# Kernel tuning notes

Hardware: AMD Instinct MI355X
Metric: run time of the kernel (lower is better)

The kernel has to match this reference:

```python
import jax, jax.numpy as jnp
import numpy as np

D_MODEL = 1024
N_HEADS = 16
D_K = D_MODEL // N_HEADS
B, S = 4, 2048


def setup_inputs() -> dict:
    key = jax.random.key(0)
    ks = jax.random.split(key, 9)
    sc = 1.0 / np.sqrt(D_MODEL)
    return {
        "x": jax.random.normal(ks[0], (B, S, D_MODEL), dtype=jnp.float32),
        "Wq": jax.random.normal(ks[1], (D_MODEL, D_MODEL), dtype=jnp.float32) * sc,
        "bq": jax.random.normal(ks[2], (D_MODEL,), dtype=jnp.float32) * 0.02,
        "Wk": jax.random.normal(ks[3], (D_MODEL, D_MODEL), dtype=jnp.float32) * sc,
        "bk": jax.random.normal(ks[4], (D_MODEL,), dtype=jnp.float32) * 0.02,
        "Wv": jax.random.normal(ks[5], (D_MODEL, D_MODEL), dtype=jnp.float32) * sc,
        "bv": jax.random.normal(ks[6], (D_MODEL,), dtype=jnp.float32) * 0.02,
        "Wo": jax.random.normal(ks[7], (D_MODEL, D_MODEL), dtype=jnp.float32) * sc,
        "bo": jax.random.normal(ks[8], (D_MODEL,), dtype=jnp.float32) * 0.02,
    }


def reference(x, Wq, bq, Wk, bk, Wv, bv, Wo, bo):
    b, s, _ = x.shape
    # QKV projections (torch Linear: x @ W.T + b; here weights are stored as [in, out])
    q = (x @ Wq + bq).reshape(b, s, N_HEADS, D_K).transpose(0, 2, 1, 3)  # [b,h,s,dk]
    k = (x @ Wk + bk).reshape(b, s, N_HEADS, D_K).transpose(0, 2, 1, 3)
    v = (x @ Wv + bv).reshape(b, s, N_HEADS, D_K).transpose(0, 2, 1, 3)
    scores = jnp.einsum("bhqd,bhkd->bhqk", q, k) / jnp.sqrt(jnp.float32(D_K))
    attn = jax.nn.softmax(scores, axis=-1)  # dropout=0.0 -> identity
    out = jnp.einsum("bhqk,bhkd->bhqd", attn, v)
    out = out.transpose(0, 2, 1, 3).reshape(b, s, D_MODEL)
    return out @ Wo + bo
```

## Files before the change

### kernel.cpp

```cpp
#include <hip/hip_runtime.h>
#include <hip/hip_bf16.h>

#define DM    1024
#define NH    16
#define DKH   64
#define BB    4
#define SS    2048
#define MROWS (BB*SS)
#define NQK   2048

typedef __attribute__((ext_vector_type(8))) __bf16 bf16x8;
typedef __attribute__((ext_vector_type(4))) float f32x4;
typedef __attribute__((ext_vector_type(4))) unsigned short u16x4;

__device__ __forceinline__ void gload_lds16(const void* g, void* l) {
  __builtin_amdgcn_global_load_lds((const __attribute__((address_space(1))) void*)g,
                                   (__attribute__((address_space(3))) void*)l, 16, 0, 0);
}

__device__ __forceinline__ unsigned short f2bf(float f) {
  __hip_bfloat16 h = __float2bfloat16(f);
  unsigned short u;
  __builtin_memcpy(&u, &h, 2);
  return u;
}


__global__ __launch_bounds__(256) void cvt_bf16_kernel(const float* __restrict__ in,
                                                       unsigned short* __restrict__ out, int n4) {
  int i = blockIdx.x * 256 + threadIdx.x;
  if (i >= n4) return;
  float4 v = reinterpret_cast<const float4*>(in)[i];
  u16x4 o = { f2bf(v.x), f2bf(v.y), f2bf(v.z), f2bf(v.w) };
  reinterpret_cast<u16x4*>(out)[i] = o;
}

__global__ __launch_bounds__(256) void transpose_cvt_kernel(const float* __restrict__ W,
                                                            unsigned short* __restrict__ WT) {
  __shared__ float t[32][33];
  int tx = threadIdx.x & 31, ty = threadIdx.x >> 5;
  int bx = blockIdx.x * 32, by = blockIdx.y * 32;
#pragma unroll
  for (int i = 0; i < 32; i += 8)
    t[ty + i][tx] = W[(long)(by + ty + i) * DM + bx + tx];
  __syncthreads();
#pragma unroll
  for (int i = 0; i < 32; i += 8)
    WT[(long)(bx + ty + i) * DM + by + tx] = f2bf(t[tx][ty + i]);
}

__global__ void concat2_bias_kernel(const float* __restrict__ a, const float* __restrict__ b,
                                    float* __restrict__ out) {
  int i = blockIdx.x * 256 + threadIdx.x;
  if (i >= NQK) return;
  out[i] = (i < DM) ? a[i] : b[i - DM];
}


__device__ __forceinline__ void store_out(float* p, float v) { *p = v; }
__device__ __forceinline__ void store_out(unsigned short* p, float v) { *p = f2bf(v); }

template <typename OutT, bool Q_SCALE, bool BIAS_ROW>
__global__ __launch_bounds__(256) void gemm_bt_kernel(
    const unsigned short* __restrict__ A,
    const unsigned short* __restrict__ BT,
    const float* __restrict__ bias,
    OutT* __restrict__ C, int M, int N, int K) {
  __shared__ unsigned short As[128 * 32];
  __shared__ unsigned short Bs[128 * 32];
  const int tid = threadIdx.x;
  const int lane = tid & 63;
  const int lr = lane & 15, lg = lane >> 4;
  const int wv = tid >> 6, wm = wv >> 1, wn = wv & 1;
  const long bm = blockIdx.x, bn = blockIdx.y;

  const unsigned short* Ag = A + bm * 128 * K;
  const unsigned short* Bg = BT + bn * 128 * K;

  f32x4 acc[4][4];
#pragma unroll
  for (int i = 0; i < 4; ++i)
#pragma unroll
    for (int j = 0; j < 4; ++j) acc[i][j] = (f32x4){0.f, 0.f, 0.f, 0.f};

  for (int kt = 0; kt < K; kt += 32) {
#pragma unroll
    for (int it = 0; it < 2; ++it) {
      const int e = it * 2048 + tid * 8;
      const int row = e >> 5, col = e & 31;
      gload_lds16(Ag + (long)row * K + kt + col, As + e);
      gload_lds16(Bg + (long)row * K + kt + col, Bs + e);
    }
    __syncthreads();
    bf16x8 af[4], bfr[4];
#pragma unroll
    for (int mi = 0; mi < 4; ++mi)
      af[mi] = *reinterpret_cast<const bf16x8*>(As + (wm * 64 + mi * 16 + lr) * 32 + lg * 8);
#pragma unroll
    for (int ni = 0; ni < 4; ++ni)
      bfr[ni] = *reinterpret_cast<const bf16x8*>(Bs + (wn * 64 + ni * 16 + lr) * 32 + lg * 8);
#pragma unroll
    for (int mi = 0; mi < 4; ++mi)
#pragma unroll
      for (int ni = 0; ni < 4; ++ni)
        acc[mi][ni] = __builtin_amdgcn_mfma_f32_16x16x32_bf16(af[mi], bfr[ni], acc[mi][ni], 0, 0, 0);
    __syncthreads();
  }

#pragma unroll
  for (int ni = 0; ni < 4; ++ni) {
    const int col = (int)bn * 128 + wn * 64 + ni * 16 + lr;
    const float bc = BIAS_ROW ? 0.f : bias[col];
    const float sc = (Q_SCALE && col < DM) ? (0.125f * 1.44269504088896340736f) : 1.0f;
#pragma unroll
    for (int mi = 0; mi < 4; ++mi) {
      const long row0 = bm * 128 + wm * 64 + mi * 16 + lg * 4;
#pragma unroll
      for (int r = 0; r < 4; ++r) {
        const float bv = BIAS_ROW ? bias[row0 + r] : bc;
        float v = (acc[mi][ni][r] + bv) * sc;
        store_out(&C[(row0 + r) * (long)N + col], v);
      }
    }
  }
}


__global__ __launch_bounds__(256) void attn_kernel(
    const unsigned short* __restrict__ QK,
    const unsigned short* __restrict__ Vt,
    unsigned short* __restrict__ AO) {
  __shared__ unsigned short Ks[2][64 * 64];
  __shared__ unsigned short Vs[2][64 * 64];
  __shared__ unsigned short Pl[4][16 * 64];

  const int tid = threadIdx.x;
  const int lane = tid & 63;
  const int wv = tid >> 6;
  const int lr = lane & 15, lg = lane >> 4;

  const int bh = blockIdx.x;
  const int qt = blockIdx.y;
  const int b = bh >> 4, h = bh & 15;

  const unsigned short* Qp = QK + (long)b * SS * NQK + h * DKH;
  const unsigned short* Kp = Qp + DM;
  const unsigned short* Vp = Vt + (long)h * DKH * MROWS + (long)b * SS;

  bf16x8 qf[2][2];
#pragma unroll
  for (int f = 0; f < 2; ++f) {
    const unsigned short* qrow = Qp + (long)(qt * 128 + wv * 32 + f * 16 + lr) * NQK;
    qf[f][0] = *reinterpret_cast<const bf16x8*>(qrow + lg * 8);
    qf[f][1] = *reinterpret_cast<const bf16x8*>(qrow + 32 + lg * 8);
  }

  f32x4 acc[2][4];
#pragma unroll
  for (int f = 0; f < 2; ++f)
#pragma unroll
    for (int d = 0; d < 4; ++d) acc[f][d] = (f32x4){0.f, 0.f, 0.f, 0.f};
  float m_run[2] = {-1e30f, -1e30f};
  float l_run[2] = {0.f, 0.f};

  unsigned short* Pw = &Pl[wv][0];

  auto stage = [&](int bf, int t) {
#pragma unroll
    for (int it = 0; it < 2; ++it) {
      const int s = it * 256 + tid;
      const int row = s >> 3, blk = s & 7;
      const int blkL = blk ^ (row & 7);
      gload_lds16(Kp + (long)(t * 64 + row) * NQK + (blkL << 3), &Ks[bf][s * 8]);
      gload_lds16(Vp + (long)row * MROWS + t * 64 + (blkL << 3), &Vs[bf][s * 8]);
    }
  };

  stage(0, 0);
  __syncthreads();

  const int NT = SS / 64;
  for (int kt = 0; kt < NT; ++kt) {
    const int cur = kt & 1;
    if (kt + 1 < NT) stage(cur ^ 1, kt + 1);

    f32x4 s4[2][4];
#pragma unroll
    for (int f = 0; f < 2; ++f)
#pragma unroll
      for (int kb = 0; kb < 4; ++kb) s4[f][kb] = (f32x4){0.f, 0.f, 0.f, 0.f};
    __builtin_amdgcn_s_setprio(1);
#pragma unroll
    for (int kb = 0; kb < 4; ++kb) {
      const unsigned short* kbase = &Ks[cur][(kb * 16 + lr) * 64];
      bf16x8 kf0 = *reinterpret_cast<const bf16x8*>(kbase + ((lg ^ (lr & 7)) << 3));
      bf16x8 kf1 = *reinterpret_cast<const bf16x8*>(kbase + (((4 + lg) ^ (lr & 7)) << 3));
      s4[0][kb] = __builtin_amdgcn_mfma_f32_16x16x32_bf16(kf0, qf[0][0], s4[0][kb], 0, 0, 0);
      s4[0][kb] = __builtin_amdgcn_mfma_f32_16x16x32_bf16(kf1, qf[0][1], s4[0][kb], 0, 0, 0);
      s4[1][kb] = __builtin_amdgcn_mfma_f32_16x16x32_bf16(kf0, qf[1][0], s4[1][kb], 0, 0, 0);
      s4[1][kb] = __builtin_amdgcn_mfma_f32_16x16x32_bf16(kf1, qf[1][1], s4[1][kb], 0, 0, 0);
    }
    __builtin_amdgcn_s_setprio(0);

    bf16x8 pf[2][2];
    float scl[2];
#pragma unroll
    for (int f = 0; f < 2; ++f) {
      float mloc = s4[f][0][0];
#pragma unroll
      for (int kb = 0; kb < 4; ++kb)
#pragma unroll
        for (int r = 0; r < 4; ++r) mloc = fmaxf(mloc, s4[f][kb][r]);
      mloc = fmaxf(mloc, __shfl_xor(mloc, 16));
      mloc = fmaxf(mloc, __shfl_xor(mloc, 32));
      const float mn = fmaxf(m_run[f], mloc);
      scl[f] = __builtin_amdgcn_exp2f(m_run[f] - mn);
      m_run[f] = mn;
      float ssum = 0.f;
#pragma unroll
      for (int kb = 0; kb < 4; ++kb) {
        u16x4 pw;
#pragma unroll
        for (int r = 0; r < 4; ++r) {
          float p = __builtin_amdgcn_exp2f(s4[f][kb][r] - mn);
          ssum += p;
          pw[r] = f2bf(p);
        }
        *reinterpret_cast<u16x4*>(Pw + lr * 64 + ((((kb * 4 + lg) ^ ((lr & 7) << 1))) << 2)) = pw;
      }
      ssum += __shfl_xor(ssum, 16);
      ssum += __shfl_xor(ssum, 32);
      l_run[f] = l_run[f] * scl[f] + ssum;
      pf[f][0] = *reinterpret_cast<const bf16x8*>(Pw + lr * 64 + (((lg * 2) ^ ((lr & 7) << 1)) << 2));
      pf[f][1] = *reinterpret_cast<const bf16x8*>(Pw + lr * 64 + (((8 + lg * 2) ^ ((lr & 7) << 1)) << 2));
    }

#pragma unroll
    for (int f = 0; f < 2; ++f)
#pragma unroll
      for (int d = 0; d < 4; ++d)
#pragma unroll
        for (int r = 0; r < 4; ++r) acc[f][d][r] *= scl[f];

    __builtin_amdgcn_s_setprio(1);
#pragma unroll
    for (int dblk = 0; dblk < 4; ++dblk) {
      const unsigned short* vbase = &Vs[cur][(dblk * 16 + lr) * 64];
      bf16x8 vf0 = *reinterpret_cast<const bf16x8*>(vbase + ((lg ^ (lr & 7)) << 3));
      bf16x8 vf1 = *reinterpret_cast<const bf16x8*>(vbase + (((4 + lg) ^ (lr & 7)) << 3));
      acc[0][dblk] = __builtin_amdgcn_mfma_f32_16x16x32_bf16(vf0, pf[0][0], acc[0][dblk], 0, 0, 0);
      acc[0][dblk] = __builtin_amdgcn_mfma_f32_16x16x32_bf16(vf1, pf[0][1], acc[0][dblk], 0, 0, 0);
      acc[1][dblk] = __builtin_amdgcn_mfma_f32_16x16x32_bf16(vf0, pf[1][0], acc[1][dblk], 0, 0, 0);
      acc[1][dblk] = __builtin_amdgcn_mfma_f32_16x16x32_bf16(vf1, pf[1][1], acc[1][dblk], 0, 0, 0);
    }
    __builtin_amdgcn_s_setprio(0);

    __syncthreads();
  }

#pragma unroll
  for (int f = 0; f < 2; ++f) {
    const float inv = 1.0f / l_run[f];
    const long row = (long)b * SS + qt * 128 + wv * 32 + f * 16 + lr;
#pragma unroll
    for (int dblk = 0; dblk < 4; ++dblk) {
      u16x4 o;
#pragma unroll
      for (int r = 0; r < 4; ++r) o[r] = f2bf(acc[f][dblk][r] * inv);
      *reinterpret_cast<u16x4*>(AO + row * DM + h * DKH + dblk * 16 + lg * 4) = o;
    }
  }
}


extern "C" void kernel_launch(void* const* d_in, const int* in_sizes, int n_in,
                              void* d_out, int out_size, void* d_ws, size_t ws_size,
                              hipStream_t stream) {
  const float* x  = (const float*)d_in[0];
  const float* Wq = (const float*)d_in[1];
  const float* bq = (const float*)d_in[2];
  const float* Wk = (const float*)d_in[3];
  const float* bk = (const float*)d_in[4];
  const float* Wv = (const float*)d_in[5];
  const float* bv = (const float*)d_in[6];
  const float* Wo = (const float*)d_in[7];
  const float* bo = (const float*)d_in[8];
  float* out = (float*)d_out;

  char* ws = (char*)d_ws;
  size_t off = 0;
  auto alloc = [&](size_t bytes) {
    void* p = ws + off;
    off += (bytes + 255) & ~(size_t)255;
    return p;
  };
  unsigned short* Xb   = (unsigned short*)alloc((size_t)MROWS * DM * 2);
  unsigned short* WTqk = (unsigned short*)alloc((size_t)2 * DM * DM * 2);
  unsigned short* WTv  = (unsigned short*)alloc((size_t)DM * DM * 2);
  unsigned short* WTo  = (unsigned short*)alloc((size_t)DM * DM * 2);
  float*          bqk  = (float*)alloc((size_t)NQK * 4);
  unsigned short* QKb  = (unsigned short*)alloc((size_t)MROWS * NQK * 2);
  unsigned short* Vtb  = (unsigned short*)alloc((size_t)DM * MROWS * 2);
  unsigned short* AOb  = (unsigned short*)alloc((size_t)MROWS * DM * 2);

  cvt_bf16_kernel<<<(MROWS * DM / 4 + 255) / 256, 256, 0, stream>>>(x, Xb, MROWS * DM / 4);
  transpose_cvt_kernel<<<dim3(32, 32), 256, 0, stream>>>(Wq, WTqk);
  transpose_cvt_kernel<<<dim3(32, 32), 256, 0, stream>>>(Wk, WTqk + DM * DM);
  transpose_cvt_kernel<<<dim3(32, 32), 256, 0, stream>>>(Wv, WTv);
  transpose_cvt_kernel<<<dim3(32, 32), 256, 0, stream>>>(Wo, WTo);
  concat2_bias_kernel<<<(NQK + 255) / 256, 256, 0, stream>>>(bq, bk, bqk);

  gemm_bt_kernel<unsigned short, true, false><<<dim3(MROWS / 128, NQK / 128), 256, 0, stream>>>(
      Xb, WTqk, bqk, QKb, MROWS, NQK, DM);
  gemm_bt_kernel<unsigned short, false, true><<<dim3(DM / 128, MROWS / 128), 256, 0, stream>>>(
      WTv, Xb, bv, Vtb, DM, MROWS, DM);

  attn_kernel<<<dim3(BB * NH, SS / 128), 256, 0, stream>>>(QKb, Vtb, AOb);

  gemm_bt_kernel<float, false, false><<<dim3(MROWS / 128, DM / 128), 256, 0, stream>>>(
      AOb, WTo, bo, out, MROWS, DM, DM);
}
```

Measured before the change: 259.3 us.

## Switch attention to 32x32x16 MFMA with register-shuffled P and lazy rescale

Rewrites the attention inner loop around 32x32x16 bf16 MFMAs instead of 16x16x32. The P tile is passed from the QK^T output layout to the PV operand layout with cross-lane shuffles rather than a round trip through LDS. K/V tiles are now stored in LDS in a k-major block layout with no XOR swizzle. Rescaling of the accumulator is skipped unless the row max grows by more than a threshold, which removes most per-tile rescale work but lets exp values grow up to 2^8 before normalization.

```diff
diff --git a/kernel.cpp b/kernel.cpp
--- a/kernel.cpp
+++ b/kernel.cpp
@@ -11,6 +11,7 @@
 
 typedef __attribute__((ext_vector_type(8))) __bf16 bf16x8;
 typedef __attribute__((ext_vector_type(4))) float f32x4;
+typedef __attribute__((ext_vector_type(16))) float f32x16;
 typedef __attribute__((ext_vector_type(4))) unsigned short u16x4;
 
 __device__ __forceinline__ void gload_lds16(const void* g, void* l) {
@@ -23,6 +24,10 @@
   unsigned short u;
   __builtin_memcpy(&u, &h, 2);
   return u;
+}
+
+__device__ __forceinline__ unsigned pack2(float a, float b) {
+  return (unsigned)f2bf(a) | ((unsigned)f2bf(b) << 16);
 }
 
 
@@ -130,14 +135,15 @@
     const unsigned short* __restrict__ QK,
     const unsigned short* __restrict__ Vt,
     unsigned short* __restrict__ AO) {
-  __shared__ unsigned short Ks[2][64 * 64];
-  __shared__ unsigned short Vs[2][64 * 64];
-  __shared__ unsigned short Pl[4][16 * 64];
+  __shared__ __align__(16) unsigned char smem[32768];
+  unsigned short* KsB = (unsigned short*)smem;
+  unsigned short* VsB = (unsigned short*)(smem + 16384);
 
   const int tid = threadIdx.x;
   const int lane = tid & 63;
   const int wv = tid >> 6;
-  const int lr = lane & 15, lg = lane >> 4;
+  const int q5 = lane & 31;
+  const int hi = lane >> 5;
 
   const int bh = blockIdx.x;
   const int qt = blockIdx.y;
@@ -147,32 +153,29 @@
   const unsigned short* Kp = Qp + DM;
   const unsigned short* Vp = Vt + (long)h * DKH * MROWS + (long)b * SS;
 
-  bf16x8 qf[2][2];
-#pragma unroll
-  for (int f = 0; f < 2; ++f) {
-    const unsigned short* qrow = Qp + (long)(qt * 128 + wv * 32 + f * 16 + lr) * NQK;
-    qf[f][0] = *reinterpret_cast<const bf16x8*>(qrow + lg * 8);
-    qf[f][1] = *reinterpret_cast<const bf16x8*>(qrow + 32 + lg * 8);
+  bf16x8 qf[4];
+  {
+    const unsigned short* qrow = Qp + (long)(qt * 128 + wv * 32 + q5) * NQK;
+#pragma unroll
+    for (int dstep = 0; dstep < 4; ++dstep)
+      qf[dstep] = *reinterpret_cast<const bf16x8*>(qrow + dstep * 16 + hi * 8);
   }
 
-  f32x4 acc[2][4];
-#pragma unroll
-  for (int f = 0; f < 2; ++f)
-#pragma unroll
-    for (int d = 0; d < 4; ++d) acc[f][d] = (f32x4){0.f, 0.f, 0.f, 0.f};
-  float m_run[2] = {-1e30f, -1e30f};
-  float l_run[2] = {0.f, 0.f};
-
-  unsigned short* Pw = &Pl[wv][0];
-
-  auto stage = [&](int bf, int t) {
+  f32x16 accv[2];
+#pragma unroll
+  for (int d = 0; d < 2; ++d)
+#pragma unroll
+    for (int r = 0; r < 16; ++r) accv[d][r] = 0.f;
+  float m_run = -1e30f, l_run = 0.f;
+
+  auto stage = [&](int buf, int t) {
+    unsigned short* kd = KsB + buf * 4096;
+    unsigned short* vd = VsB + buf * 4096;
 #pragma unroll
     for (int it = 0; it < 2; ++it) {
-      const int s = it * 256 + tid;
-      const int row = s >> 3, blk = s & 7;
-      const int blkL = blk ^ (row & 7);
-      gload_lds16(Kp + (long)(t * 64 + row) * NQK + (blkL << 3), &Ks[bf][s * 8]);
-      gload_lds16(Vp + (long)row * MROWS + t * 64 + (blkL << 3), &Vs[bf][s * 8]);
+      const int u = it * 256 + tid;
+      gload_lds16(Kp + (long)(t * 64 + (u & 63)) * NQK + (u >> 6) * 8, kd + u * 8);
+      gload_lds16(Vp + (long)(u & 63) * MROWS + t * 64 + (u >> 6) * 8, vd + u * 8);
     }
   };
 
@@ -183,93 +186,98 @@
   for (int kt = 0; kt < NT; ++kt) {
     const int cur = kt & 1;
     if (kt + 1 < NT) stage(cur ^ 1, kt + 1);
-
-    f32x4 s4[2][4];
-#pragma unroll
-    for (int f = 0; f < 2; ++f)
-#pragma unroll
-      for (int kb = 0; kb < 4; ++kb) s4[f][kb] = (f32x4){0.f, 0.f, 0.f, 0.f};
+    const unsigned short* K_ = KsB + cur * 4096;
+    const unsigned short* V_ = VsB + cur * 4096;
+
+    f32x16 s4[2];
+#pragma unroll
+    for (int kb = 0; kb < 2; ++kb)
+#pragma unroll
+      for (int r = 0; r < 16; ++r) s4[kb][r] = 0.f;
     __builtin_amdgcn_s_setprio(1);
 #pragma unroll
-    for (int kb = 0; kb < 4; ++kb) {
-      const unsigned short* kbase = &Ks[cur][(kb * 16 + lr) * 64];
-      bf16x8 kf0 = *reinterpret_cast<const bf16x8*>(kbase + ((lg ^ (lr & 7)) << 3));
-      bf16x8 kf1 = *reinterpret_cast<const bf16x8*>(kbase + (((4 + lg) ^ (lr & 7)) << 3));
-      s4[0][kb] = __builtin_amdgcn_mfma_f32_16x16x32_bf16(kf0, qf[0][0], s4[0][kb], 0, 0, 0);
-      s4[0][kb] = __builtin_amdgcn_mfma_f32_16x16x32_bf16(kf1, qf[0][1], s4[0][kb], 0, 0, 0);
-      s4[1][kb] = __builtin_amdgcn_mfma_f32_16x16x32_bf16(kf0, qf[1][0], s4[1][kb], 0, 0, 0);
-      s4[1][kb] = __builtin_amdgcn_mfma_f32_16x16x32_bf16(kf1, qf[1][1], s4[1][kb], 0, 0, 0);
-    }
+    for (int kb = 0; kb < 2; ++kb)
+#pragma unroll
+      for (int dstep = 0; dstep < 4; ++dstep) {
+        bf16x8 kf = *reinterpret_cast<const bf16x8*>(
+            K_ + ((dstep * 2 + hi) * 64 + kb * 32 + q5) * 8);
+        s4[kb] = __builtin_amdgcn_mfma_f32_32x32x16_bf16(kf, qf[dstep], s4[kb], 0, 0, 0);
+      }
     __builtin_amdgcn_s_setprio(0);
 
-    bf16x8 pf[2][2];
-    float scl[2];
-#pragma unroll
-    for (int f = 0; f < 2; ++f) {
-      float mloc = s4[f][0][0];
-#pragma unroll
-      for (int kb = 0; kb < 4; ++kb)
-#pragma unroll
-        for (int r = 0; r < 4; ++r) mloc = fmaxf(mloc, s4[f][kb][r]);
-      mloc = fmaxf(mloc, __shfl_xor(mloc, 16));
-      mloc = fmaxf(mloc, __shfl_xor(mloc, 32));
-      const float mn = fmaxf(m_run[f], mloc);
-      scl[f] = __builtin_amdgcn_exp2f(m_run[f] - mn);
-      m_run[f] = mn;
-      float ssum = 0.f;
-#pragma unroll
-      for (int kb = 0; kb < 4; ++kb) {
-        u16x4 pw;
-#pragma unroll
-        for (int r = 0; r < 4; ++r) {
-          float p = __builtin_amdgcn_exp2f(s4[f][kb][r] - mn);
-          ssum += p;
-          pw[r] = f2bf(p);
-        }
-        *reinterpret_cast<u16x4*>(Pw + lr * 64 + ((((kb * 4 + lg) ^ ((lr & 7) << 1))) << 2)) = pw;
+    float tmax[16];
+#pragma unroll
+    for (int r = 0; r < 16; ++r) tmax[r] = fmaxf(s4[0][r], s4[1][r]);
+#pragma unroll
+    for (int w = 8; w >= 1; w >>= 1)
+#pragma unroll
+      for (int r = 0; r < w; ++r) tmax[r] = fmaxf(tmax[r], tmax[r + w]);
+    const float mloc = fmaxf(tmax[0], __shfl_xor(tmax[0], 32));
+
+    if (!__all(mloc <= m_run + 8.0f)) {
+      const float mn = fmaxf(m_run, mloc);
+      const float scl = __builtin_amdgcn_exp2f(m_run - mn);
+      m_run = mn;
+      l_run *= scl;
+#pragma unroll
+      for (int d = 0; d < 2; ++d)
+#pragma unroll
+        for (int r = 0; r < 16; ++r) accv[d][r] *= scl;
+    }
+
+#pragma unroll
+    for (int kb = 0; kb < 2; ++kb)
+#pragma unroll
+      for (int r = 0; r < 16; ++r)
+        s4[kb][r] = __builtin_amdgcn_exp2f(s4[kb][r] - m_run);
+    float tsum[16];
+#pragma unroll
+    for (int r = 0; r < 16; ++r) tsum[r] = s4[0][r] + s4[1][r];
+#pragma unroll
+    for (int w = 8; w >= 1; w >>= 1)
+#pragma unroll
+      for (int r = 0; r < w; ++r) tsum[r] += tsum[r + w];
+    l_run += tsum[0] + __shfl_xor(tsum[0], 32);
+
+#pragma unroll
+    for (int step = 0; step < 4; ++step) {
+      const int kb = step >> 1, rb = (step & 1) * 8;
+      const unsigned w0 = pack2(s4[kb][rb + 0], s4[kb][rb + 1]);
+      const unsigned w1 = pack2(s4[kb][rb + 2], s4[kb][rb + 3]);
+      const unsigned w2 = pack2(s4[kb][rb + 4], s4[kb][rb + 5]);
+      const unsigned w3 = pack2(s4[kb][rb + 6], s4[kb][rb + 7]);
+      const unsigned x0 = (unsigned)__shfl_xor((int)w0, 32);
+      const unsigned x1 = (unsigned)__shfl_xor((int)w1, 32);
+      const unsigned x2 = (unsigned)__shfl_xor((int)w2, 32);
+      const unsigned x3 = (unsigned)__shfl_xor((int)w3, 32);
+      union { unsigned u[4]; bf16x8 v; } pf;
+      pf.u[0] = hi ? x2 : w0;
+      pf.u[1] = hi ? x3 : w1;
+      pf.u[2] = hi ? w2 : x0;
+      pf.u[3] = hi ? w3 : x1;
+      __builtin_amdgcn_s_setprio(1);
+#pragma unroll
+      for (int dblk = 0; dblk < 2; ++dblk) {
+        bf16x8 vf = *reinterpret_cast<const bf16x8*>(
+            V_ + ((step * 2 + hi) * 64 + dblk * 32 + q5) * 8);
+        accv[dblk] = __builtin_amdgcn_mfma_f32_32x32x16_bf16(vf, pf.v, accv[dblk], 0, 0, 0);
       }
-      ssum += __shfl_xor(ssum, 16);
-      ssum += __shfl_xor(ssum, 32);
-      l_run[f] = l_run[f] * scl[f] + ssum;
-      pf[f][0] = *reinterpret_cast<const bf16x8*>(Pw + lr * 64 + (((lg * 2) ^ ((lr & 7) << 1)) << 2));
-      pf[f][1] = *reinterpret_cast<const bf16x8*>(Pw + lr * 64 + (((8 + lg * 2) ^ ((lr & 7) << 1)) << 2));
-    }
-
-#pragma unroll
-    for (int f = 0; f < 2; ++f)
-#pragma unroll
-      for (int d = 0; d < 4; ++d)
-#pragma unroll
-        for (int r = 0; r < 4; ++r) acc[f][d][r] *= scl[f];
-
-    __builtin_amdgcn_s_setprio(1);
-#pragma unroll
-    for (int dblk = 0; dblk < 4; ++dblk) {
-      const unsigned short* vbase = &Vs[cur][(dblk * 16 + lr) * 64];
-      bf16x8 vf0 = *reinterpret_cast<const bf16x8*>(vbase + ((lg ^ (lr & 7)) << 3));
-      bf16x8 vf1 = *reinterpret_cast<const bf16x8*>(vbase + (((4 + lg) ^ (lr & 7)) << 3));
-      acc[0][dblk] = __builtin_amdgcn_mfma_f32_16x16x32_bf16(vf0, pf[0][0], acc[0][dblk], 0, 0, 0);
-      acc[0][dblk] = __builtin_amdgcn_mfma_f32_16x16x32_bf16(vf1, pf[0][1], acc[0][dblk], 0, 0, 0);
-      acc[1][dblk] = __builtin_amdgcn_mfma_f32_16x16x32_bf16(vf0, pf[1][0], acc[1][dblk], 0, 0, 0);
-      acc[1][dblk] = __builtin_amdgcn_mfma_f32_16x16x32_bf16(vf1, pf[1][1], acc[1][dblk], 0, 0, 0);
-    }
-    __builtin_amdgcn_s_setprio(0);
-
+      __builtin_amdgcn_s_setprio(0);
+    }
     __syncthreads();
   }
 
-#pragma unroll
-  for (int f = 0; f < 2; ++f) {
-    const float inv = 1.0f / l_run[f];
-    const long row = (long)b * SS + qt * 128 + wv * 32 + f * 16 + lr;
-#pragma unroll
-    for (int dblk = 0; dblk < 4; ++dblk) {
-      u16x4 o;
-#pragma unroll
-      for (int r = 0; r < 4; ++r) o[r] = f2bf(acc[f][dblk][r] * inv);
-      *reinterpret_cast<u16x4*>(AO + row * DM + h * DKH + dblk * 16 + lg * 4) = o;
-    }
-  }
+  const float inv = 1.0f / l_run;
+  const long row = (long)b * SS + qt * 128 + wv * 32 + q5;
+  unsigned short* orow = AO + row * DM + h * DKH;
+#pragma unroll
+  for (int dblk = 0; dblk < 2; ++dblk)
+#pragma unroll
+    for (int j = 0; j < 8; ++j) {
+      const int d0 = dblk * 32 + 8 * (j >> 1) + 4 * hi + 2 * (j & 1);
+      const unsigned w = pack2(accv[dblk][2 * j] * inv, accv[dblk][2 * j + 1] * inv);
+      *reinterpret_cast<unsigned*>(orow + d0) = w;
+    }
 }
 
 
```

Result: slower. 270.0 us (+4.1%).
